# Performance work log

Measured on AMD Instinct MI355X. Metric: run time of the kernel, lower is better.

## Reference

```python
import jax, jax.numpy as jnp
import numpy as np

RES = 32          # resolution (32, 32) -> N = 1024 tokens
HEADS = 16
EMB = 1024
BATCH = 8
N = RES * RES


def _bias_idxs(res):
    # relative-offset index table, [N, N] with values in [0, res*res)
    coords = np.stack(np.meshgrid(np.arange(res), np.arange(res), indexing='ij'), -1).reshape(-1, 2)
    d = np.abs(coords[:, None, :] - coords[None, :, :])  # [N, N, 2]
    return jnp.asarray(d[..., 0] * res + d[..., 1], dtype=jnp.int64)


def setup_inputs() -> dict:
    key = jax.random.key(0)
    k1, k2, k3, k4, k5 = jax.random.split(key, 5)
    x = jax.random.normal(k1, (BATCH, N, EMB), dtype=jnp.float32)
    w_qkv = jax.random.normal(k2, (3 * EMB, EMB), dtype=jnp.float32) * 0.02
    biases = jax.random.normal(k3, (HEADS, RES * RES), dtype=jnp.float32) * 0.02
    bias_idxs = _bias_idxs(RES)
    w_out = jax.random.normal(k4, (EMB, EMB), dtype=jnp.float32) * 0.02
    b_out = jax.random.normal(k5, (EMB,), dtype=jnp.float32) * 0.02
    return {"x": x, "w_qkv": w_qkv, "biases": biases,
            "bias_idxs": bias_idxs, "w_out": w_out, "b_out": b_out}


def reference(x, w_qkv, biases, bias_idxs, w_out, b_out):
    b, n, e = x.shape
    h = HEADS
    d = e // h
    scale = d ** -0.5
    # to_qkv: Linear(e, 3e, bias=False); torch Linear computes x @ W.T
    qkv = x @ w_qkv.T                                   # [b, n, 3e]
    q, k, v = jnp.split(qkv, 3, axis=-1)
    def to_heads(t):
        return t.reshape(b, n, h, d).transpose(0, 2, 1, 3)  # b h n d
    q, k, v = to_heads(q), to_heads(k), to_heads(v)
    scores = jnp.einsum('bhid,bhjd->bhij', q, k) * scale    # [b, h, n, n]
    scores = scores + biases[:, bias_idxs]                  # gather -> [h, n, n], broadcast over b
    attn = jax.nn.softmax(scores, axis=-1)
    out = jnp.einsum('bhij,bhjd->bhid', attn, v)            # [b, h, n, d]
    out = out.transpose(0, 2, 1, 3).reshape(b, n, e)        # b n (h d)
    # to_out: Linear(e, e) with bias (dropout = identity at inference)
    return out @ w_out.T + b_out
```

## Files before the change

### kernel.cpp

```cpp
#include <hip/hip_runtime.h>
#include <stdint.h>


#define LOG2E 1.4426950408889634f

typedef __attribute__((ext_vector_type(8))) short short8;
typedef __attribute__((ext_vector_type(4))) short short4v;
typedef __attribute__((ext_vector_type(4))) float floatx4;
typedef __attribute__((ext_vector_type(2))) unsigned int uint2v;

__device__ __forceinline__ short f2bf(float f) {
  uint32_t u = __builtin_bit_cast(uint32_t, f);
  u = (u + 0x7FFFu + ((u >> 16) & 1u)) >> 16;
  return (short)(uint16_t)u;
}
__device__ __forceinline__ float bf2f(short s) {
  uint32_t u = ((uint32_t)(uint16_t)s) << 16;
  return __builtin_bit_cast(float, u);
}
__device__ __forceinline__ float fast_exp2(float x) {
#if __has_builtin(__builtin_amdgcn_exp2f)
  return __builtin_amdgcn_exp2f(x);
#else
  return exp2f(x);
#endif
}

__device__ __forceinline__ void gload_lds16(const short* g, short* l) {
  __builtin_amdgcn_global_load_lds(
      (const __attribute__((address_space(1))) void*)g,
      (__attribute__((address_space(3))) void*)l, 16, 0, 0);
}

__global__ void cvt_bf16(const float* __restrict__ src, short* __restrict__ dst, int n4) {
  int i = blockIdx.x * 256 + threadIdx.x;
  if (i >= n4) return;
  float4 f = ((const float4*)src)[i];
  short4v o;
  o.x = f2bf(f.x); o.y = f2bf(f.y); o.z = f2bf(f.z); o.w = f2bf(f.w);
  ((short4v*)dst)[i] = o;
}

__global__ void bias_precomp(const float* __restrict__ biases, short* __restrict__ biast) {
  int t = blockIdx.x * 256 + threadIdx.x;
  int lane = t & 63;
  int tile = t >> 6;
  int jt = tile & 63, it = (tile >> 6) & 63, h = tile >> 12;
  int i0 = it * 16 + ((lane >> 4) << 2);
  int j = jt * 16 + (lane & 15);
  int rj = j >> 5, cj = j & 31;
  short4v o;
#pragma unroll
  for (int r = 0; r < 4; r++) {
    int i = i0 + r;
    int ri = i >> 5, ci = i & 31;
    int dr = ri - rj; if (dr < 0) dr = -dr;
    int dc = ci - cj; if (dc < 0) dc = -dc;
    o[r] = f2bf(biases[h * 1024 + dr * 32 + dc] * LOG2E);
  }
  *(short4v*)&biast[(size_t)t * 4] = o;
}

template <int MODE>
__global__ __launch_bounds__(256, 2) void gemm_bt(
    const short* __restrict__ A, const short* __restrict__ Bt,
    short* __restrict__ qo, short* __restrict__ ko, short* __restrict__ vto,
    const float* __restrict__ bvec, float* __restrict__ outf) {
  __shared__ __align__(16) short sA[128 * 64];
  __shared__ __align__(16) short sB[128 * 64];
  const int tid = threadIdx.x;
  const int w = tid >> 6, lane = tid & 63;
  const int wr = w >> 1, wc = w & 1;
  const int bm = blockIdx.y, bn = blockIdx.x;
  const int qd = lane >> 4, col = lane & 15;

  floatx4 acc[4][4] = {};
  const int rowA0 = bm * 128, rowB0 = bn * 128;
  const int ciw = w * 256;

  for (int kk = 0; kk < 1024; kk += 64) {
    __syncthreads();
#pragma unroll
    for (int n = 0; n < 4; n++) {
      int ci = ciw + n * 64 + lane;
      int r = ci >> 3, c = (ci & 7) ^ (r & 7);
      gload_lds16(A + (size_t)(rowA0 + r) * 1024 + kk + c * 8, &sA[ci * 8]);
    }
#pragma unroll
    for (int n = 0; n < 4; n++) {
      int ci = ciw + n * 64 + lane;
      int r = ci >> 3, c = (ci & 7) ^ (r & 7);
      gload_lds16(Bt + (size_t)(rowB0 + r) * 1024 + kk + c * 8, &sB[ci * 8]);
    }
    __syncthreads();

#pragma unroll
    for (int ks = 0; ks < 2; ks++) {
      const int ch = qd + ks * 4;
      short8 af[4], bff[4];
#pragma unroll
      for (int rt = 0; rt < 4; rt++) {
        int r = wr * 64 + rt * 16 + col;
        af[rt] = *(const short8*)&sA[r * 64 + ((ch ^ (r & 7)) << 3)];
      }
#pragma unroll
      for (int ct = 0; ct < 4; ct++) {
        int r = wc * 64 + ct * 16 + col;
        bff[ct] = *(const short8*)&sB[r * 64 + ((ch ^ (r & 7)) << 3)];
      }
#pragma unroll
      for (int rt = 0; rt < 4; rt++)
#pragma unroll
        for (int ct = 0; ct < 4; ct++)
          acc[rt][ct] = __builtin_amdgcn_mfma_f32_16x16x32_bf16(af[rt], bff[ct], acc[rt][ct], 0, 0, 0);
    }
  }

  if (MODE == 0) {
    if (bn >= 16) {
#pragma unroll
      for (int rt = 0; rt < 4; rt++) {
#pragma unroll
        for (int ct = 0; ct < 4; ct++) {
          int Cg = bn * 128 + wc * 64 + ct * 16 + col;
          int e = Cg & 1023, h = e >> 6, dd = e & 63;
          short4v pv;
#pragma unroll
          for (int r = 0; r < 4; r++) pv[r] = f2bf(acc[rt][ct][r]);
          int R0 = bm * 128 + wr * 64 + rt * 16 + qd * 4;
          int b = R0 >> 10, n0 = R0 & 1023;
          int bh = b * 16 + h;
          *(short4v*)&vto[((size_t)bh * 64 + dd) * 1024 + n0] = pv;
        }
      }
    } else {
#pragma unroll
      for (int rt = 0; rt < 4; rt++) {
#pragma unroll
        for (int ct = 0; ct < 4; ct++) {
          int Cg = bn * 128 + wc * 64 + ct * 16 + col;
          int which = Cg >> 10, e = Cg & 1023, h = e >> 6, dd = e & 63;
#pragma unroll
          for (int r = 0; r < 4; r++) {
            int R = bm * 128 + wr * 64 + rt * 16 + qd * 4 + r;
            int b = R >> 10, n = R & 1023;
            int bh = b * 16 + h;
            short v = f2bf(acc[rt][ct][r]);
            if (which == 0)
              qo[((size_t)bh * 1024 + n) * 64 + dd] = v;
            else
              ko[((size_t)bh * 1024 + n) * 64 + dd] = v;
          }
        }
      }
    }
  } else {
#pragma unroll
    for (int rt = 0; rt < 4; rt++)
#pragma unroll
      for (int ct = 0; ct < 4; ct++) {
        int Cg = bn * 128 + wc * 64 + ct * 16 + col;
        float bo = bvec[Cg];
#pragma unroll
        for (int r = 0; r < 4; r++) {
          int R = bm * 128 + wr * 64 + rt * 16 + qd * 4 + r;
          outf[(size_t)R * 1024 + Cg] = acc[rt][ct][r] + bo;
        }
      }
  }
}

__global__ __launch_bounds__(256, 3) void attn_fused(
    const short* __restrict__ q, const short* __restrict__ k,
    const short* __restrict__ vt, const short* __restrict__ biast,
    short* __restrict__ ao) {
  __shared__ __align__(16) short sPK[128 * 64];
  __shared__ __align__(16) short sVt[64 * 128];
  const int tid = threadIdx.x, w = tid >> 6, lane = tid & 63;
  const int bh = blockIdx.x, qt = blockIdx.y;
  const int h = bh & 15;
  const int qd = lane >> 4, col = lane & 15;
  const short* qb = q + (size_t)bh * 65536;
  const short* kb = k + (size_t)bh * 65536;
  const short* vb = vt + (size_t)bh * 65536;
  const int ciw = w * 256;

#pragma unroll
  for (int n = 0; n < 2; n++) {
    int ci = w * 128 + n * 64 + lane;
    int r = ci >> 3, c = (ci & 7) ^ (r & 7);
    gload_lds16(qb + (size_t)(qt * 64 + r) * 64 + c * 8, &sVt[ci * 8]);
  }
  __syncthreads();
  short8 bq[2][4];
#pragma unroll
  for (int ks = 0; ks < 2; ks++) {
    const int ch = qd + ks * 4;
#pragma unroll
    for (int ct = 0; ct < 4; ct++) {
      int r2 = ct * 16 + col;
      bq[ks][ct] = *(const short8*)&sVt[r2 * 64 + ((ch ^ (r2 & 7)) << 3)];
    }
  }

  short8 onesf;
#pragma unroll
  for (int t = 0; t < 8; t++) onesf[t] = (short)0x3F80;

  floatx4 oacc[4] = {};
  floatx4 osum = {};
  const float SCL = 0.125f * LOG2E;

  for (int js = 0; js < 8; js++) {
    __syncthreads();
#pragma unroll
    for (int n = 0; n < 4; n++) {
      int ci = ciw + n * 64 + lane;
      int r = ci >> 3, c = (ci & 7) ^ (r & 7);
      gload_lds16(kb + (size_t)(js * 128 + r) * 64 + c * 8, &sPK[ci * 8]);
    }
#pragma unroll
    for (int n = 0; n < 4; n++) {
      int ci = ciw + n * 64 + lane;
      int r = ci >> 4, c = (ci & 15) ^ (r & 15);
      gload_lds16(vb + (size_t)r * 1024 + js * 128 + c * 8, &sVt[ci * 8]);
    }
    __syncthreads();

    short8 ak[2][2];
#pragma unroll
    for (int rt = 0; rt < 2; rt++)
#pragma unroll
      for (int ks = 0; ks < 2; ks++) {
        const int ch = qd + ks * 4;
        int r = w * 32 + rt * 16 + col;
        ak[rt][ks] = *(const short8*)&sPK[r * 64 + ((ch ^ (r & 7)) << 3)];
      }
    __syncthreads();

#pragma unroll
    for (int rt = 0; rt < 2; rt++) {
      const int a = js * 8 + w * 2 + rt;
      const int s = w * 8 + rt * 4 + qd;
      short4v bfrag[4];
#pragma unroll
      for (int ct = 0; ct < 4; ct++) {
        int b = qt * 4 + ct;
        bfrag[ct] = *(const short4v*)&biast[((((size_t)h * 64 + a) * 64 + b) << 8) + lane * 4];
      }
      floatx4 sacc[4] = {};
#pragma unroll
      for (int ks = 0; ks < 2; ks++)
#pragma unroll
        for (int ct = 0; ct < 4; ct++)
          sacc[ct] = __builtin_amdgcn_mfma_f32_16x16x32_bf16(
              ak[rt][ks], bq[ks][ct], sacc[ct], 0, 0, 0);
#pragma unroll
      for (int ct = 0; ct < 4; ct++) {
        int i = ct * 16 + col;
        float e0 = fast_exp2(fmaf(sacc[ct][0], SCL, bf2f(bfrag[ct][0])));
        float e1 = fast_exp2(fmaf(sacc[ct][1], SCL, bf2f(bfrag[ct][1])));
        float e2 = fast_exp2(fmaf(sacc[ct][2], SCL, bf2f(bfrag[ct][2])));
        float e3 = fast_exp2(fmaf(sacc[ct][3], SCL, bf2f(bfrag[ct][3])));
        uint32_t u0 = __builtin_bit_cast(uint32_t, e0) + 0x8000u;
        uint32_t u1 = __builtin_bit_cast(uint32_t, e1) + 0x8000u;
        uint32_t u2 = __builtin_bit_cast(uint32_t, e2) + 0x8000u;
        uint32_t u3 = __builtin_bit_cast(uint32_t, e3) + 0x8000u;
        uint2v pk;
        pk.x = __builtin_amdgcn_perm(u1, u0, 0x07060302u);
        pk.y = __builtin_amdgcn_perm(u3, u2, 0x07060302u);
        *(uint2v*)&sPK[i * 128 + ((s ^ (i & 15)) << 2)] = pk;
      }
    }
    __syncthreads();

#pragma unroll
    for (int ks = 0; ks < 4; ks++) {
      const int ch = ks * 4 + qd;
      int m = w * 16 + col;
      short4v lo = *(const short4v*)&sPK[m * 128 + (((2 * ch) ^ col) << 2)];
      short4v hi = *(const short4v*)&sPK[m * 128 + (((2 * ch + 1) ^ col) << 2)];
      short8 ap = __builtin_shufflevector(lo, hi, 0, 1, 2, 3, 4, 5, 6, 7);
      short8 bv[4];
#pragma unroll
      for (int ct = 0; ct < 4; ct++) {
        int d = ct * 16 + col;
        bv[ct] = *(const short8*)&sVt[d * 128 + ((ch ^ (d & 15)) << 3)];
      }
#pragma unroll
      for (int ct = 0; ct < 4; ct++)
        oacc[ct] = __builtin_amdgcn_mfma_f32_16x16x32_bf16(ap, bv[ct], oacc[ct], 0, 0, 0);
      osum = __builtin_amdgcn_mfma_f32_16x16x32_bf16(ap, onesf, osum, 0, 0, 0);
    }
  }

  const int b = bh >> 4;
  floatx4 inv;
#pragma unroll
  for (int r = 0; r < 4; r++) inv[r] = 1.0f / osum[r];
#pragma unroll
  for (int ct = 0; ct < 4; ct++)
#pragma unroll
    for (int r = 0; r < 4; r++) {
      int n = qt * 64 + w * 16 + qd * 4 + r;
      int dd = ct * 16 + col;
      ao[(((size_t)b * 1024 + n) << 10) + h * 64 + dd] = f2bf(oacc[ct][r] * inv[r]);
    }
}

extern "C" void kernel_launch(void* const* d_in, const int* in_sizes, int n_in,
                              void* d_out, int out_size, void* d_ws, size_t ws_size,
                              hipStream_t stream) {
  const float* x = (const float*)d_in[0];
  const float* w_qkv = (const float*)d_in[1];
  const float* biases = (const float*)d_in[2];
  const float* w_out = (const float*)d_in[4];
  const float* b_out = (const float*)d_in[5];
  float* out = (float*)d_out;

  char* ws = (char*)d_ws;
  short* xb    = (short*)(ws + 0);
  short* wqkvb = (short*)(ws + 16777216);
  short* woutb = (short*)(ws + 23068672);
  short* qb    = (short*)(ws + 25165824);
  short* kb    = (short*)(ws + 41943040);
  short* vtb   = (short*)(ws + 58720256);
  short* aob   = (short*)(ws + 75497472);
  short* biast = (short*)(ws + 92274688);

  cvt_bf16<<<8192, 256, 0, stream>>>(x, xb, 8192 * 1024 / 4);
  cvt_bf16<<<3072, 256, 0, stream>>>(w_qkv, wqkvb, 3072 * 1024 / 4);
  cvt_bf16<<<1024, 256, 0, stream>>>(w_out, woutb, 1024 * 1024 / 4);
  bias_precomp<<<16384, 256, 0, stream>>>(biases, biast);

  gemm_bt<0><<<dim3(24, 64), 256, 0, stream>>>(xb, wqkvb, qb, kb, vtb, nullptr, nullptr);
  attn_fused<<<dim3(128, 16), 256, 0, stream>>>(qb, kb, vtb, biast, aob);
  gemm_bt<1><<<dim3(8, 64), 256, 0, stream>>>(aob, woutb, nullptr, nullptr, nullptr, b_out, out);
}
```

Before: 264.5 us.

## Double-buffer K/V tiles in LDS to prefetch the next block during compute

Splits the shared K/P and V buffers into double-buffered K and V tiles plus a separate P buffer. The next K/V tile is loaded asynchronously while the current tile's QK^T, softmax and PV are computed, which also removes one barrier per iteration. LDS use per block rises substantially, so the launch bound drops from 3 to 2 blocks per SM. Any intermediate barrier that forces the outstanding loads to finish may limit how much of the load is actually hidden.

Result: no change. 268.5 us (+1.5%).

```diff
diff --git a/kernel.cpp b/kernel.cpp
--- a/kernel.cpp
+++ b/kernel.cpp
@@ -170,12 +170,13 @@
   }
 }
 
-__global__ __launch_bounds__(256, 3) void attn_fused(
+__global__ __launch_bounds__(256, 2) void attn_fused(
     const short* __restrict__ q, const short* __restrict__ k,
     const short* __restrict__ vt, const short* __restrict__ biast,
     short* __restrict__ ao) {
-  __shared__ __align__(16) short sPK[128 * 64];
-  __shared__ __align__(16) short sVt[64 * 128];
+  __shared__ __align__(16) short sK[2][128 * 64];
+  __shared__ __align__(16) short sV[2][64 * 128];
+  __shared__ __align__(16) short sP[64 * 128];
   const int tid = threadIdx.x, w = tid >> 6, lane = tid & 63;
   const int bh = blockIdx.x, qt = blockIdx.y;
   const int h = bh & 15;
@@ -189,7 +190,19 @@
   for (int n = 0; n < 2; n++) {
     int ci = w * 128 + n * 64 + lane;
     int r = ci >> 3, c = (ci & 7) ^ (r & 7);
-    gload_lds16(qb + (size_t)(qt * 64 + r) * 64 + c * 8, &sVt[ci * 8]);
+    gload_lds16(qb + (size_t)(qt * 64 + r) * 64 + c * 8, &sP[ci * 8]);
+  }
+#pragma unroll
+  for (int n = 0; n < 4; n++) {
+    int ci = ciw + n * 64 + lane;
+    int r = ci >> 3, c = (ci & 7) ^ (r & 7);
+    gload_lds16(kb + (size_t)r * 64 + c * 8, &sK[0][ci * 8]);
+  }
+#pragma unroll
+  for (int n = 0; n < 4; n++) {
+    int ci = ciw + n * 64 + lane;
+    int r = ci >> 4, c = (ci & 15) ^ (r & 15);
+    gload_lds16(vb + (size_t)r * 1024 + c * 8, &sV[0][ci * 8]);
   }
   __syncthreads();
   short8 bq[2][4];
@@ -199,7 +212,7 @@
 #pragma unroll
     for (int ct = 0; ct < 4; ct++) {
       int r2 = ct * 16 + col;
-      bq[ks][ct] = *(const short8*)&sVt[r2 * 64 + ((ch ^ (r2 & 7)) << 3)];
+      bq[ks][ct] = *(const short8*)&sP[r2 * 64 + ((ch ^ (r2 & 7)) << 3)];
     }
   }
 
@@ -212,32 +225,24 @@
   const float SCL = 0.125f * LOG2E;
 
   for (int js = 0; js < 8; js++) {
+    const int cur = js & 1, nxt = cur ^ 1;
     __syncthreads();
-#pragma unroll
-    for (int n = 0; n < 4; n++) {
-      int ci = ciw + n * 64 + lane;
-      int r = ci >> 3, c = (ci & 7) ^ (r & 7);
-      gload_lds16(kb + (size_t)(js * 128 + r) * 64 + c * 8, &sPK[ci * 8]);
-    }
-#pragma unroll
-    for (int n = 0; n < 4; n++) {
-      int ci = ciw + n * 64 + lane;
-      int r = ci >> 4, c = (ci & 15) ^ (r & 15);
-      gload_lds16(vb + (size_t)r * 1024 + js * 128 + c * 8, &sVt[ci * 8]);
-    }
-    __syncthreads();
-
-    short8 ak[2][2];
-#pragma unroll
-    for (int rt = 0; rt < 2; rt++)
-#pragma unroll
-      for (int ks = 0; ks < 2; ks++) {
-        const int ch = qd + ks * 4;
-        int r = w * 32 + rt * 16 + col;
-        ak[rt][ks] = *(const short8*)&sPK[r * 64 + ((ch ^ (r & 7)) << 3)];
-      }
-    __syncthreads();
-
+    if (js < 7) {
+#pragma unroll
+      for (int n = 0; n < 4; n++) {
+        int ci = ciw + n * 64 + lane;
+        int r = ci >> 3, c = (ci & 7) ^ (r & 7);
+        gload_lds16(kb + (size_t)((js + 1) * 128 + r) * 64 + c * 8, &sK[nxt][ci * 8]);
+      }
+#pragma unroll
+      for (int n = 0; n < 4; n++) {
+        int ci = ciw + n * 64 + lane;
+        int r = ci >> 4, c = (ci & 15) ^ (r & 15);
+        gload_lds16(vb + (size_t)r * 1024 + (js + 1) * 128 + c * 8, &sV[nxt][ci * 8]);
+      }
+    }
+
+    const short* sKc = sK[cur];
 #pragma unroll
     for (int rt = 0; rt < 2; rt++) {
       const int a = js * 8 + w * 2 + rt;
@@ -248,13 +253,16 @@
         int b = qt * 4 + ct;
         bfrag[ct] = *(const short4v*)&biast[((((size_t)h * 64 + a) * 64 + b) << 8) + lane * 4];
       }
+      const int r = w * 32 + rt * 16 + col;
+      short8 ak0 = *(const short8*)&sKc[r * 64 + (((qd + 0) ^ (r & 7)) << 3)];
+      short8 ak1 = *(const short8*)&sKc[r * 64 + (((qd + 4) ^ (r & 7)) << 3)];
       floatx4 sacc[4] = {};
 #pragma unroll
-      for (int ks = 0; ks < 2; ks++)
-#pragma unroll
-        for (int ct = 0; ct < 4; ct++)
-          sacc[ct] = __builtin_amdgcn_mfma_f32_16x16x32_bf16(
-              ak[rt][ks], bq[ks][ct], sacc[ct], 0, 0, 0);
+      for (int ct = 0; ct < 4; ct++)
+        sacc[ct] = __builtin_amdgcn_mfma_f32_16x16x32_bf16(ak0, bq[0][ct], sacc[ct], 0, 0, 0);
+#pragma unroll
+      for (int ct = 0; ct < 4; ct++)
+        sacc[ct] = __builtin_amdgcn_mfma_f32_16x16x32_bf16(ak1, bq[1][ct], sacc[ct], 0, 0, 0);
 #pragma unroll
       for (int ct = 0; ct < 4; ct++) {
         int i = ct * 16 + col;
@@ -269,23 +277,24 @@
         uint2v pk;
         pk.x = __builtin_amdgcn_perm(u1, u0, 0x07060302u);
         pk.y = __builtin_amdgcn_perm(u3, u2, 0x07060302u);
-        *(uint2v*)&sPK[i * 128 + ((s ^ (i & 15)) << 2)] = pk;
+        *(uint2v*)&sP[i * 128 + ((s ^ (i & 15)) << 2)] = pk;
       }
     }
     __syncthreads();
 
+    const short* sVc = sV[cur];
 #pragma unroll
     for (int ks = 0; ks < 4; ks++) {
       const int ch = ks * 4 + qd;
       int m = w * 16 + col;
-      short4v lo = *(const short4v*)&sPK[m * 128 + (((2 * ch) ^ col) << 2)];
-      short4v hi = *(const short4v*)&sPK[m * 128 + (((2 * ch + 1) ^ col) << 2)];
+      short4v lo = *(const short4v*)&sP[m * 128 + (((2 * ch) ^ col) << 2)];
+      short4v hi = *(const short4v*)&sP[m * 128 + (((2 * ch + 1) ^ col) << 2)];
       short8 ap = __builtin_shufflevector(lo, hi, 0, 1, 2, 3, 4, 5, 6, 7);
       short8 bv[4];
 #pragma unroll
       for (int ct = 0; ct < 4; ct++) {
         int d = ct * 16 + col;
-        bv[ct] = *(const short8*)&sVt[d * 128 + ((ch ^ (d & 15)) << 3)];
+        bv[ct] = *(const short8*)&sVc[d * 128 + ((ch ^ (d & 15)) << 3)];
       }
 #pragma unroll
       for (int ct = 0; ct < 4; ct++)
```
